# Kernel tuning notes

Measured on AMD Instinct MI355X. Metric: run time of the kernel, lower is better.

Reference implementation:

```python
import jax, jax.numpy as jnp
import numpy as np

B, N, D = 4, 2048, 4
COUPLING = 1.0
DT = 1.0


def setup_inputs() -> dict:
    key = jax.random.key(0)
    k1, k2, k3, k4 = jax.random.split(key, 4)
    theta_prev = jax.random.normal(k1, (B, N, D), dtype=jnp.float32)
    gamma_t = jax.random.normal(k2, (B, N, D), dtype=jnp.float32)
    affinity = jax.random.uniform(k3, (B, N, N), dtype=jnp.float32)
    alpha_t = jax.random.normal(k4, (B, N, N), dtype=jnp.float32)
    # learned parameters, initialized as in the torch module
    omega = jnp.zeros((N, D), dtype=jnp.float32)
    kappa = jnp.ones((N, D), dtype=jnp.float32)
    alpha_bias = jnp.zeros((N, N), dtype=jnp.float32)
    return {
        "theta_prev": theta_prev,
        "gamma_t": gamma_t,
        "affinity": affinity,
        "alpha_t": alpha_t,
        "omega": omega,
        "kappa": kappa,
        "alpha_bias": alpha_bias,
    }


def reference(theta_prev, gamma_t, affinity, alpha_t, omega, kappa, alpha_bias):
    # theta_prev: [B, N, D], affinity/alpha_t: [B, N, N]
    n = theta_prev.shape[1]
    alpha_total = alpha_t + alpha_bias[None, :, :]               # [B, N, N]
    # phase_term[b, i, j, d] = sin(theta[b, j, d] - theta[b, i, d] - alpha_total[b, i, j])
    phase_term = jnp.sin(
        theta_prev[:, None, :, :] - theta_prev[:, :, None, :]
        - alpha_total[:, :, :, None]
    )                                                            # [B, N, N, D]
    coupling_term = (COUPLING / n) * jnp.einsum(
        "bij,bijd->bid", affinity, phase_term
    )                                                            # [B, N, D]
    drive_term = kappa[None, :, :] * (gamma_t - theta_prev)
    theta_dot = omega[None, :, :] + drive_term + coupling_term
    return theta_prev + DT * theta_dot
```

## Files before the change

### kernel.cpp

```cpp
#include <hip/hip_runtime.h>

#define BB 4
#define NN 2048
#define DD 4
#define QQ (NN / 4)
#define BLOCK 256
#define JIT (QQ / 64)

typedef float f4 __attribute__((ext_vector_type(4)));
typedef _Float16 h8 __attribute__((ext_vector_type(8)));

__global__ __launch_bounds__(BLOCK) void precomp(const float* __restrict__ theta,
                                                 float* __restrict__ sArr,
                                                 float* __restrict__ cArr,
                                                 h8* __restrict__ scT) {
    const int t = blockIdx.x * BLOCK + threadIdx.x;
    const int b = t / QQ, q = t % QQ;
    const f4* theta4 = (const f4*)theta;
    f4* s4 = (f4*)sArr;
    f4* c4 = (f4*)cArr;

    float s[4][4], c[4][4];
    #pragma unroll
    for (int u = 0; u < 4; ++u) {
        const f4 th = theta4[(size_t)b * NN + 4 * q + u];
        #pragma unroll
        for (int d = 0; d < 4; ++d) __sincosf(th[d], &s[u][d], &c[u][d]);
    }
    #pragma unroll
    for (int u = 0; u < 4; ++u) {
        f4 sv, cv;
        #pragma unroll
        for (int d = 0; d < 4; ++d) { sv[d] = s[u][d]; cv[d] = c[u][d]; }
        s4[(size_t)b * NN + 4 * q + u] = sv;
        c4[(size_t)b * NN + 4 * q + u] = cv;
    }
    #pragma unroll
    for (int d = 0; d < 4; ++d) {
        h8 w;
        #pragma unroll
        for (int u = 0; u < 4; ++u) {
            w[2 * u]     = (_Float16)s[u][d];
            w[2 * u + 1] = (_Float16)c[u][d];
        }
        scT[((size_t)b * 4 + d) * QQ + q] = w;
    }
}

__global__ __launch_bounds__(BLOCK, 5) void kuramoto_main(
    const float* __restrict__ theta,
    const float* __restrict__ gam,
    const float* __restrict__ aff,
    const float* __restrict__ alp,
    const float* __restrict__ omega,
    const float* __restrict__ kappa,
    const float* __restrict__ bias,
    const float* __restrict__ sArr,
    const float* __restrict__ cArr,
    const h8* __restrict__ scT,
    float* __restrict__ out)
{
    const int x   = blockIdx.x;
    const int low = x & 31;
    const int b   = low >> 3;
    const int g   = (x >> 5) * 8 + (low & 7);
    const int i0  = g * 4;

    const int tid  = threadIdx.x;
    const int wave = tid >> 6;
    const int lane = tid & 63;
    const int i    = i0 + wave;

    __shared__ h8 lsc[4 * QQ];
    {
        const h8* gsc = scT + (size_t)b * 4 * QQ;
        #pragma unroll
        for (int k = 0; k < (4 * QQ) / BLOCK; ++k)
            lsc[tid + BLOCK * k] = gsc[tid + BLOCK * k];
    }
    __syncthreads();

    const f4* arow = (const f4*)(aff + (size_t)b * NN * NN) + (size_t)i * QQ;
    const f4* lrow = (const f4*)(alp + (size_t)b * NN * NN) + (size_t)i * QQ;
    const f4* brow = (const f4*)bias + (size_t)i * QQ;

    f4 accU = {0.f, 0.f, 0.f, 0.f};
    f4 accV = {0.f, 0.f, 0.f, 0.f};

    f4 av[2], lv[2], bv[2];
    av[0] = __builtin_nontemporal_load(&arow[lane]);
    lv[0] = __builtin_nontemporal_load(&lrow[lane]);
    bv[0] = brow[lane];

    #pragma unroll
    for (int jj = 0; jj < JIT; ++jj) {
        const int cur = jj & 1;
        const int nxt = cur ^ 1;
        const int q   = lane + 64 * jj;

        if (jj + 1 < JIT) {
            const int qn = q + 64;
            av[nxt] = __builtin_nontemporal_load(&arow[qn]);
            lv[nxt] = __builtin_nontemporal_load(&lrow[qn]);
            bv[nxt] = brow[qn];
        }

        f4 sj[4], cj[4];
        #pragma unroll
        for (int d = 0; d < 4; ++d) {
            const h8 w = lsc[d * QQ + q];
            #pragma unroll
            for (int u = 0; u < 4; ++u) {
                sj[u][d] = (float)w[2 * u];
                cj[u][d] = (float)w[2 * u + 1];
            }
        }

        const f4 alr = lv[cur] + bv[cur];
        const f4 af  = av[cur];
        #pragma unroll
        for (int u = 0; u < 4; ++u) {
            float sa, ca;
            __sincosf(alr[u], &sa, &ca);
            const float wc = af[u] * ca;
            const float ws = af[u] * sa;
            accU += wc * sj[u] - ws * cj[u];
            accV += wc * cj[u] + ws * sj[u];
        }
    }

    #pragma unroll
    for (int off = 32; off >= 1; off >>= 1) {
        #pragma unroll
        for (int d = 0; d < 4; ++d) {
            accU[d] += __shfl_down(accU[d], off, 64);
            accV[d] += __shfl_down(accV[d], off, 64);
        }
    }

    if (lane == 0) {
        const f4* theta4 = (const f4*)theta;
        const f4* gam4   = (const f4*)gam;
        const f4* om4    = (const f4*)omega;
        const f4* kp4    = (const f4*)kappa;
        const f4* s4     = (const f4*)sArr;
        const f4* c4     = (const f4*)cArr;
        f4* out4         = (f4*)out;

        const size_t base = (size_t)b * NN + i;
        const f4 th = theta4[base];
        const f4 gm = gam4[base];
        const f4 om = om4[i];
        const f4 kp = kp4[i];
        const f4 si = s4[base];
        const f4 ci = c4[base];
        f4 o;
        #pragma unroll
        for (int d = 0; d < 4; ++d) {
            const float coup = (1.0f / (float)NN) * (ci[d] * accU[d] - si[d] * accV[d]);
            o[d] = th[d] + om[d] + kp[d] * (gm[d] - th[d]) + coup;
        }
        out4[base] = o;
    }
}

extern "C" void kernel_launch(void* const* d_in, const int* in_sizes, int n_in,
                              void* d_out, int out_size, void* d_ws, size_t ws_size,
                              hipStream_t stream) {
    const float* theta = (const float*)d_in[0];
    const float* gam   = (const float*)d_in[1];
    const float* aff   = (const float*)d_in[2];
    const float* alp   = (const float*)d_in[3];
    const float* omega = (const float*)d_in[4];
    const float* kappa = (const float*)d_in[5];
    const float* bias  = (const float*)d_in[6];
    float* out  = (float*)d_out;

    float* sArr = (float*)d_ws;
    float* cArr = sArr + BB * NN * DD;
    h8*    scT  = (h8*)(cArr + BB * NN * DD);

    precomp<<<(BB * QQ) / BLOCK, BLOCK, 0, stream>>>(theta, sArr, cArr, scT);
    kuramoto_main<<<BB * (NN / 4), BLOCK, 0, stream>>>(
        theta, gam, aff, alp, omega, kappa, bias, sArr, cArr, scT, out);
}
```

Baseline: 169.6 us.

## Drop LDS staging, deepen prefetch, use packed fp16 dot2 for coupling accumulation

Removes the shared-memory copy of the sin/cos table and the block barrier, and instead loads the per-batch fp16 sin/cos entries directly from global memory (L2-resident) with a one-step prefetch. It deepens the affinity/alpha streaming prefetch to two iterations ahead with a triple buffer and changes block-to-row mapping to simple batch-major order. The inner accumulation converts the weighted sin/cos pair to packed fp16 and uses fdot2 instructions to halve the FMA count. In exchange, the weights are rounded toward zero to fp16, which reduces accuracy, and register pressure rises.

```diff
diff --git a/kernel.cpp b/kernel.cpp
--- a/kernel.cpp
+++ b/kernel.cpp
@@ -9,6 +9,7 @@
 
 typedef float f4 __attribute__((ext_vector_type(4)));
 typedef _Float16 h8 __attribute__((ext_vector_type(8)));
+typedef _Float16 h2 __attribute__((ext_vector_type(2)));
 
 __global__ __launch_bounds__(BLOCK) void precomp(const float* __restrict__ theta,
                                                  float* __restrict__ sArr,
@@ -60,72 +61,82 @@
     const h8* __restrict__ scT,
     float* __restrict__ out)
 {
-    const int x   = blockIdx.x;
-    const int low = x & 31;
-    const int b   = low >> 3;
-    const int g   = (x >> 5) * 8 + (low & 7);
-    const int i0  = g * 4;
+    const int x = blockIdx.x;
+    const int b = x >> 9;
+    const int g = x & 511;
 
     const int tid  = threadIdx.x;
     const int wave = tid >> 6;
     const int lane = tid & 63;
-    const int i    = i0 + wave;
-
-    __shared__ h8 lsc[4 * QQ];
-    {
-        const h8* gsc = scT + (size_t)b * 4 * QQ;
-        #pragma unroll
-        for (int k = 0; k < (4 * QQ) / BLOCK; ++k)
-            lsc[tid + BLOCK * k] = gsc[tid + BLOCK * k];
-    }
-    __syncthreads();
+    const int i    = g * 4 + wave;
 
     const f4* arow = (const f4*)(aff + (size_t)b * NN * NN) + (size_t)i * QQ;
     const f4* lrow = (const f4*)(alp + (size_t)b * NN * NN) + (size_t)i * QQ;
     const f4* brow = (const f4*)bias + (size_t)i * QQ;
+    const h8* scp  = scT + (size_t)b * 4 * QQ;
 
     f4 accU = {0.f, 0.f, 0.f, 0.f};
     f4 accV = {0.f, 0.f, 0.f, 0.f};
 
-    f4 av[2], lv[2], bv[2];
+    f4 av[3], lv[3];
+    f4 bv[2];
+    h8 sc[2][4];
+
     av[0] = __builtin_nontemporal_load(&arow[lane]);
     lv[0] = __builtin_nontemporal_load(&lrow[lane]);
+    av[1] = __builtin_nontemporal_load(&arow[lane + 64]);
+    lv[1] = __builtin_nontemporal_load(&lrow[lane + 64]);
     bv[0] = brow[lane];
+    #pragma unroll
+    for (int d = 0; d < 4; ++d) sc[0][d] = scp[d * QQ + lane];
 
     #pragma unroll
     for (int jj = 0; jj < JIT; ++jj) {
         const int cur = jj & 1;
         const int nxt = cur ^ 1;
-        const int q   = lane + 64 * jj;
+        const int s0  = jj % 3;
 
+        if (jj + 2 < JIT) {
+            const int qn = lane + 64 * (jj + 2);
+            av[(jj + 2) % 3] = __builtin_nontemporal_load(&arow[qn]);
+            lv[(jj + 2) % 3] = __builtin_nontemporal_load(&lrow[qn]);
+        }
         if (jj + 1 < JIT) {
-            const int qn = q + 64;
-            av[nxt] = __builtin_nontemporal_load(&arow[qn]);
-            lv[nxt] = __builtin_nontemporal_load(&lrow[qn]);
+            const int qn = lane + 64 * (jj + 1);
             bv[nxt] = brow[qn];
+            #pragma unroll
+            for (int d = 0; d < 4; ++d) sc[nxt][d] = scp[d * QQ + qn];
         }
 
-        f4 sj[4], cj[4];
-        #pragma unroll
-        for (int d = 0; d < 4; ++d) {
-            const h8 w = lsc[d * QQ + q];
-            #pragma unroll
-            for (int u = 0; u < 4; ++u) {
-                sj[u][d] = (float)w[2 * u];
-                cj[u][d] = (float)w[2 * u + 1];
-            }
-        }
+        const f4 af  = av[s0];
+        const f4 alr = lv[s0] + bv[cur];
 
-        const f4 alr = lv[cur] + bv[cur];
-        const f4 af  = av[cur];
         #pragma unroll
         for (int u = 0; u < 4; ++u) {
             float sa, ca;
             __sincosf(alr[u], &sa, &ca);
             const float wc = af[u] * ca;
             const float ws = af[u] * sa;
-            accU += wc * sj[u] - ws * cj[u];
-            accV += wc * cj[u] + ws * sj[u];
+#if __has_builtin(__builtin_amdgcn_cvt_pkrtz) && __has_builtin(__builtin_amdgcn_fdot2)
+            const h2 hA = __builtin_bit_cast(h2, __builtin_amdgcn_cvt_pkrtz(wc, -ws));
+            const h2 hB = __builtin_bit_cast(h2, __builtin_amdgcn_cvt_pkrtz(ws, wc));
+            #pragma unroll
+            for (int d = 0; d < 4; ++d) {
+                h2 p;
+                p[0] = sc[cur][d][2 * u];
+                p[1] = sc[cur][d][2 * u + 1];
+                accU[d] = __builtin_amdgcn_fdot2(hA, p, accU[d], false);
+                accV[d] = __builtin_amdgcn_fdot2(hB, p, accV[d], false);
+            }
+#else
+            #pragma unroll
+            for (int d = 0; d < 4; ++d) {
+                const float sj = (float)sc[cur][d][2 * u];
+                const float cj = (float)sc[cur][d][2 * u + 1];
+                accU[d] = fmaf(wc, sj, fmaf(-ws, cj, accU[d]));
+                accV[d] = fmaf(wc, cj, fmaf(ws, sj, accV[d]));
+            }
+#endif
         }
     }
 
```

Result: no change. 172.4 us (+1.7%).
